# Kernel optimization log

Measured on AMD Instinct MI355X. Metric: run time of the kernel, lower is better.

## Reference

```python
import jax, jax.numpy as jnp
import numpy as np

C_CH, S_DIM, H_DIM, RANK = 256, 16, 128, 8


def setup_inputs() -> dict:
    key = jax.random.key(0)
    k = jax.random.split(key, 6)
    x = jax.random.normal(k[0], (1, C_CH, S_DIM, H_DIM, H_DIM), dtype=jnp.float32)
    # Conv1d(kernel=1, bias=False) weights per rank; kaiming-ish fan_out scaling
    W1 = jax.random.normal(k[1], (RANK, C_CH, C_CH), jnp.float32) * np.sqrt(2.0 / C_CH)
    W2 = jax.random.normal(k[2], (RANK, S_DIM, S_DIM), jnp.float32) * np.sqrt(2.0 / S_DIM)
    W3 = jax.random.normal(k[3], (RANK, H_DIM, H_DIM), jnp.float32) * np.sqrt(2.0 / H_DIM)
    W4 = jax.random.normal(k[4], (RANK, H_DIM, H_DIM), jnp.float32) * np.sqrt(2.0 / H_DIM)
    lam = jnp.ones((RANK,), dtype=jnp.float32)
    return {"x": x, "W1": W1, "W2": W2, "W3": W3, "W4": W4, "lam": lam}


def reference(x, W1, W2, W3, W4, lam):
    # x: (1, c, s, w, h); AdaptiveAvgPool3d(1) on permuted views == global means
    Cv = x.mean(axis=(0, 2, 3, 4))  # (c,)  channel pooling
    Sv = x.mean(axis=(0, 1, 3, 4))  # (s,)
    Hv = x.mean(axis=(0, 1, 2, 3))  # (h,)  last spatial dim
    Wv = x.mean(axis=(0, 1, 2, 4))  # (w,)

    # original detaches softmax(lam) and always uses index 0
    lam_sm = jax.lax.stop_gradient(jax.nn.softmax(lam))
    coef = lam_sm[0]

    # per-rank 1x1 conv + sigmoid == sigmoid(W @ v), batched over rank
    cf = jax.nn.sigmoid(jnp.einsum('rij,j->ri', W1, Cv))  # (r, c)
    sf = jax.nn.sigmoid(jnp.einsum('rij,j->ri', W2, Sv))  # (r, s)
    hf = jax.nn.sigmoid(jnp.einsum('rij,j->ri', W3, Hv))  # (r, h)
    wf = jax.nn.sigmoid(jnp.einsum('rij,j->ri', W4, Wv))  # (r, w)

    # chained bmm with ps=1 == rank-1 outer product, summed over rank
    tensor1 = coef * jnp.einsum('rc,rs,rh,rw->cshw', cf, sf, hf, wf)
    tensor1 = tensor1[None]  # (1, c, s, h, w) matching x layout

    return jnp.concatenate([x, jax.nn.relu(x * tensor1)], axis=1)
```

## Files before the change

kernel.cpp:

```cpp
#include <hip/hip_runtime.h>

typedef float f32x4 __attribute__((ext_vector_type(4)));

#define C_CH 256
#define S_DIM 16
#define HW 128
#define RANK 8
#define NCOPY 16

#define OFF_PC 0
#define OFF_PS 4096
#define OFF_PI 4352
#define OFF_PJ 6400
#define OFF_CF 8448
#define OFF_SF 10496
#define OFF_HF 10624
#define OFF_WF 11648

__global__ __launch_bounds__(256) void k_init(float* __restrict__ ws) {
    int idx = blockIdx.x * 256 + threadIdx.x;
    if (idx < OFF_CF) ws[idx] = 0.f;
}

__global__ __launch_bounds__(256) void k_reduce(const float* __restrict__ x,
                                                float* __restrict__ out,
                                                float* __restrict__ ws) {
    int b = blockIdx.x;
    int c = b >> 2;
    int s0 = (b & 3) * 4;
    int t = threadIdx.x;
    int lane = t & 31;
    int rg = t >> 5;
    int j0 = lane * 4;

    float colacc[4] = {0.f, 0.f, 0.f, 0.f};
    float rowacc[16] = {0.f};
    float tot[4] = {0.f, 0.f, 0.f, 0.f};

    for (int q = 0; q < 4; ++q) {
        size_t slab = (size_t)(b * 4 + q) * 16384;
        const f32x4* xs = reinterpret_cast<const f32x4*>(x + slab);
        f32x4* o1 = reinterpret_cast<f32x4*>(out + slab);
#pragma unroll
        for (int k = 0; k < 16; ++k) {
            f32x4 v = xs[k * 256 + t];
            __builtin_nontemporal_store(v, &o1[k * 256 + t]);
            colacc[0] += v.x; colacc[1] += v.y;
            colacc[2] += v.z; colacc[3] += v.w;
            float s4 = (v.x + v.y) + (v.z + v.w);
            rowacc[k] += s4;
            tot[q] += s4;
        }
    }

    __shared__ float ldsr[128 * 33];
    __shared__ float ldsc[128 * 9];
    __shared__ float ldst[4][4];

#pragma unroll
    for (int k = 0; k < 16; ++k) ldsr[(k * 8 + rg) * 33 + lane] = rowacc[k];
#pragma unroll
    for (int jj = 0; jj < 4; ++jj) ldsc[(j0 + jj) * 9 + rg] = colacc[jj];
#pragma unroll
    for (int q = 0; q < 4; ++q) {
        float v = tot[q];
        for (int d = 32; d > 0; d >>= 1) v += __shfl_down(v, d, 64);
        if ((t & 63) == 0) ldst[t >> 6][q] = v;
    }
    __syncthreads();

    int copy = b & (NCOPY - 1);
    if (t < 128) {
        float rsum = 0.f;
#pragma unroll
        for (int l = 0; l < 32; ++l) rsum += ldsr[t * 33 + l];
        atomicAdd(&ws[OFF_PI + copy * 128 + t], rsum);
    } else {
        int j = t - 128;
        float csum = 0.f;
#pragma unroll
        for (int g = 0; g < 8; ++g) csum += ldsc[j * 9 + g];
        atomicAdd(&ws[OFF_PJ + copy * 128 + j], csum);
    }
    if (t < 4) {
        float sv = ldst[0][t] + ldst[1][t] + ldst[2][t] + ldst[3][t];
        atomicAdd(&ws[OFF_PS + copy * 16 + s0 + t], sv);
    }
    if (t == 8) {
        float cv = 0.f;
#pragma unroll
        for (int w = 0; w < 4; ++w)
#pragma unroll
            for (int q = 0; q < 4; ++q) cv += ldst[w][q];
        atomicAdd(&ws[OFF_PC + copy * 256 + c], cv);
    }
}

__global__ __launch_bounds__(256) void k_factors(const float* __restrict__ W1,
                                                 const float* __restrict__ W2,
                                                 const float* __restrict__ W3,
                                                 const float* __restrict__ W4,
                                                 const float* __restrict__ lam,
                                                 float* __restrict__ ws) {
    __shared__ float mC[256], mS[16], mW[128], mH[128];
    int t = threadIdx.x;
    for (int idx = t; idx < 528; idx += 256) {
        float acc = 0.f;
        if (idx < 256) {
            for (int cp = 0; cp < NCOPY; ++cp) acc += ws[OFF_PC + cp * 256 + idx];
            mC[idx] = acc * (1.f / (S_DIM * 16384.f));
        } else if (idx < 272) {
            int q = idx - 256;
            for (int cp = 0; cp < NCOPY; ++cp) acc += ws[OFF_PS + cp * 16 + q];
            mS[q] = acc * (1.f / (C_CH * 16384.f));
        } else if (idx < 400) {
            int q = idx - 272;
            for (int cp = 0; cp < NCOPY; ++cp) acc += ws[OFF_PI + cp * 128 + q];
            mW[q] = acc * (1.f / (C_CH * S_DIM * 128.f));
        } else {
            int q = idx - 400;
            for (int cp = 0; cp < NCOPY; ++cp) acc += ws[OFF_PJ + cp * 128 + q];
            mH[q] = acc * (1.f / (C_CH * S_DIM * 128.f));
        }
    }
    __syncthreads();

    float m = lam[0];
    for (int r = 1; r < RANK; ++r) m = fmaxf(m, lam[r]);
    float den = 0.f;
    for (int r = 0; r < RANK; ++r) den += expf(lam[r] - m);
    float coef = expf(lam[0] - m) / den;

    int rid = blockIdx.x * 256 + t;
    if (rid < 2048) {
        int r = rid >> 8, i = rid & 255;
        const float* w = W1 + r * 65536 + i * 256;
        float d = 0.f;
        for (int k = 0; k < 256; ++k) d += w[k] * mC[k];
        ws[OFF_CF + rid] = coef / (1.f + expf(-d));
    } else if (rid < 2176) {
        int q = rid - 2048;
        int r = q >> 4, i = q & 15;
        const float* w = W2 + r * 256 + i * 16;
        float d = 0.f;
        for (int k = 0; k < 16; ++k) d += w[k] * mS[k];
        ws[OFF_SF + q] = 1.f / (1.f + expf(-d));
    } else if (rid < 3200) {
        int q = rid - 2176;
        int r = q >> 7, i = q & 127;
        const float* w = W3 + r * 16384 + i * 128;
        float d = 0.f;
        for (int k = 0; k < 128; ++k) d += w[k] * mH[k];
        ws[OFF_HF + q] = 1.f / (1.f + expf(-d));
    } else if (rid < 4224) {
        int q = rid - 3200;
        int r = q >> 7, i = q & 127;
        const float* w = W4 + r * 16384 + i * 128;
        float d = 0.f;
        for (int k = 0; k < 128; ++k) d += w[k] * mW[k];
        ws[OFF_WF + q] = 1.f / (1.f + expf(-d));
    }
}

__global__ __launch_bounds__(256) void k_output(const float* __restrict__ x,
                                                const float* __restrict__ ws,
                                                float* __restrict__ out) {
    int b = blockIdx.x;
    int c = b >> 4, s = b & 15;
    int t = threadIdx.x;

    __shared__ float hb[128 * 8];
    __shared__ float wb[128 * 8];

    const float* cf = ws + OFF_CF;
    const float* sf = ws + OFF_SF;
    const float* hf = ws + OFF_HF;
    const float* wf = ws + OFF_WF;

    for (int idx = t; idx < 1024; idx += 256) {
        int r = idx & 7, p = idx >> 3;
        hb[idx] = hf[r * 128 + p];
        wb[idx] = cf[r * 256 + c] * sf[r * 16 + s] * wf[r * 128 + p];
    }
    __syncthreads();

    int j0 = (t & 31) * 4, rg = t >> 5;
    float wreg[4][8];
#pragma unroll
    for (int jj = 0; jj < 4; ++jj)
#pragma unroll
        for (int r = 0; r < 8; ++r) wreg[jj][r] = wb[(j0 + jj) * 8 + r];

    size_t slab = (size_t)b * 16384;
    const f32x4* xs = reinterpret_cast<const f32x4*>(x + slab);
    f32x4* o2 = reinterpret_cast<f32x4*>(out + (size_t)67108864 + slab);

    for (int k = 0; k < 16; ++k) {
        int i = k * 8 + rg;
        int vidx = i * 32 + (t & 31);
        f32x4 v = xs[vidx];
        float h[8];
#pragma unroll
        for (int r = 0; r < 8; ++r) h[r] = hb[i * 8 + r];
        float t0 = 0.f, t1 = 0.f, t2 = 0.f, t3 = 0.f;
#pragma unroll
        for (int r = 0; r < 8; ++r) {
            t0 += h[r] * wreg[0][r];
            t1 += h[r] * wreg[1][r];
            t2 += h[r] * wreg[2][r];
            t3 += h[r] * wreg[3][r];
        }
        f32x4 y;
        y.x = fmaxf(v.x * t0, 0.f);
        y.y = fmaxf(v.y * t1, 0.f);
        y.z = fmaxf(v.z * t2, 0.f);
        y.w = fmaxf(v.w * t3, 0.f);
        __builtin_nontemporal_store(y, &o2[vidx]);
    }
}

extern "C" void kernel_launch(void* const* d_in, const int* in_sizes, int n_in,
                              void* d_out, int out_size, void* d_ws, size_t ws_size,
                              hipStream_t stream) {
    const float* x   = (const float*)d_in[0];
    const float* W1  = (const float*)d_in[1];
    const float* W2  = (const float*)d_in[2];
    const float* W3  = (const float*)d_in[3];
    const float* W4  = (const float*)d_in[4];
    const float* lam = (const float*)d_in[5];
    float* ws  = (float*)d_ws;
    float* out = (float*)d_out;

    k_init<<<33, 256, 0, stream>>>(ws);
    k_reduce<<<1024, 256, 0, stream>>>(x, out, ws);
    k_factors<<<17, 256, 0, stream>>>(W1, W2, W3, W4, lam, ws);
    k_output<<<4096, 256, 0, stream>>>(x, ws, out);
}
```

Measured before the change: 195.8 us.

## Stage bf16 copy of input in workspace for the gated-output pass

After: 193.2 us (median of 2 runs). No clear change (-1.3%).

```diff
diff --git a/kernel.cpp b/kernel.cpp
--- a/kernel.cpp
+++ b/kernel.cpp
@@ -1,6 +1,7 @@
 #include <hip/hip_runtime.h>
 
 typedef float f32x4 __attribute__((ext_vector_type(4)));
+typedef unsigned short u16x4 __attribute__((ext_vector_type(4)));
 
 #define C_CH 256
 #define S_DIM 16
@@ -16,12 +17,21 @@
 #define OFF_SF 10496
 #define OFF_HF 10624
 #define OFF_WF 11648
+#define OFF_BF 16384
+
+#define BF_WS_BYTES ((size_t)65536 + (size_t)67108864 * 2)
+
+__device__ __forceinline__ unsigned short bf16rne(float f) {
+    unsigned u = __float_as_uint(f);
+    return (unsigned short)((u + 0x7FFFu + ((u >> 16) & 1u)) >> 16);
+}
 
 __global__ __launch_bounds__(256) void k_init(float* __restrict__ ws) {
     int idx = blockIdx.x * 256 + threadIdx.x;
     if (idx < OFF_CF) ws[idx] = 0.f;
 }
 
+template <bool WBF>
 __global__ __launch_bounds__(256) void k_reduce(const float* __restrict__ x,
                                                 float* __restrict__ out,
                                                 float* __restrict__ ws) {
@@ -33,6 +43,9 @@
     int rg = t >> 5;
     int j0 = lane * 4;
 
+    u16x4* bfp = reinterpret_cast<u16x4*>(
+        reinterpret_cast<unsigned short*>(ws + OFF_BF));
+
     float colacc[4] = {0.f, 0.f, 0.f, 0.f};
     float rowacc[16] = {0.f};
     float tot[4] = {0.f, 0.f, 0.f, 0.f};
@@ -41,10 +54,19 @@
         size_t slab = (size_t)(b * 4 + q) * 16384;
         const f32x4* xs = reinterpret_cast<const f32x4*>(x + slab);
         f32x4* o1 = reinterpret_cast<f32x4*>(out + slab);
+        u16x4* bf = bfp + (slab >> 2);
 #pragma unroll
         for (int k = 0; k < 16; ++k) {
-            f32x4 v = xs[k * 256 + t];
+            f32x4 v = __builtin_nontemporal_load(&xs[k * 256 + t]);
             __builtin_nontemporal_store(v, &o1[k * 256 + t]);
+            if (WBF) {
+                u16x4 hv;
+                hv.x = bf16rne(v.x);
+                hv.y = bf16rne(v.y);
+                hv.z = bf16rne(v.z);
+                hv.w = bf16rne(v.w);
+                bf[k * 256 + t] = hv;
+            }
             colacc[0] += v.x; colacc[1] += v.y;
             colacc[2] += v.z; colacc[3] += v.w;
             float s4 = (v.x + v.y) + (v.z + v.w);
@@ -162,9 +184,8 @@
     }
 }
 
-__global__ __launch_bounds__(256) void k_output(const float* __restrict__ x,
-                                                const float* __restrict__ ws,
-                                                float* __restrict__ out) {
+__global__ __launch_bounds__(256) void k_output_bf(const float* __restrict__ ws,
+                                                   float* __restrict__ out) {
     int b = blockIdx.x;
     int c = b >> 4, s = b & 15;
     int t = threadIdx.x;
@@ -191,14 +212,20 @@
 #pragma unroll
         for (int r = 0; r < 8; ++r) wreg[jj][r] = wb[(j0 + jj) * 8 + r];
 
-    size_t slab = (size_t)b * 16384;
-    const f32x4* xs = reinterpret_cast<const f32x4*>(x + slab);
-    f32x4* o2 = reinterpret_cast<f32x4*>(out + (size_t)67108864 + slab);
+    const u16x4* bf = reinterpret_cast<const u16x4*>(
+        reinterpret_cast<const unsigned short*>(ws + OFF_BF));
+    size_t slab4 = (size_t)b * 4096;
+    f32x4* o2 = reinterpret_cast<f32x4*>(out + (size_t)67108864 + (size_t)b * 16384);
 
     for (int k = 0; k < 16; ++k) {
         int i = k * 8 + rg;
         int vidx = i * 32 + (t & 31);
-        f32x4 v = xs[vidx];
+        u16x4 hv = bf[slab4 + vidx];
+        f32x4 v;
+        v.x = __uint_as_float((unsigned)hv.x << 16);
+        v.y = __uint_as_float((unsigned)hv.y << 16);
+        v.z = __uint_as_float((unsigned)hv.z << 16);
+        v.w = __uint_as_float((unsigned)hv.w << 16);
         float h[8];
 #pragma unroll
         for (int r = 0; r < 8; ++r) h[r] = hb[i * 8 + r];
@@ -219,6 +246,63 @@
     }
 }
 
+__global__ __launch_bounds__(256) void k_output_fp(const float* __restrict__ x,
+                                                   const float* __restrict__ ws,
+                                                   float* __restrict__ out) {
+    int b = blockIdx.x;
+    int c = b >> 4, s = b & 15;
+    int t = threadIdx.x;
+
+    __shared__ float hb[128 * 8];
+    __shared__ float wb[128 * 8];
+
+    const float* cf = ws + OFF_CF;
+    const float* sf = ws + OFF_SF;
+    const float* hf = ws + OFF_HF;
+    const float* wf = ws + OFF_WF;
+
+    for (int idx = t; idx < 1024; idx += 256) {
+        int r = idx & 7, p = idx >> 3;
+        hb[idx] = hf[r * 128 + p];
+        wb[idx] = cf[r * 256 + c] * sf[r * 16 + s] * wf[r * 128 + p];
+    }
+    __syncthreads();
+
+    int j0 = (t & 31) * 4, rg = t >> 5;
+    float wreg[4][8];
+#pragma unroll
+    for (int jj = 0; jj < 4; ++jj)
+#pragma unroll
+        for (int r = 0; r < 8; ++r) wreg[jj][r] = wb[(j0 + jj) * 8 + r];
+
+    size_t slab = (size_t)b * 16384;
+    const f32x4* xs = reinterpret_cast<const f32x4*>(x + slab);
+    f32x4* o2 = reinterpret_cast<f32x4*>(out + (size_t)67108864 + slab);
+
+    for (int k = 0; k < 16; ++k) {
+        int i = k * 8 + rg;
+        int vidx = i * 32 + (t & 31);
+        f32x4 v = xs[vidx];
+        float h[8];
+#pragma unroll
+        for (int r = 0; r < 8; ++r) h[r] = hb[i * 8 + r];
+        float t0 = 0.f, t1 = 0.f, t2 = 0.f, t3 = 0.f;
+#pragma unroll
+        for (int r = 0; r < 8; ++r) {
+            t0 += h[r] * wreg[0][r];
+            t1 += h[r] * wreg[1][r];
+            t2 += h[r] * wreg[2][r];
+            t3 += h[r] * wreg[3][r];
+        }
+        f32x4 y;
+        y.x = fmaxf(v.x * t0, 0.f);
+        y.y = fmaxf(v.y * t1, 0.f);
+        y.z = fmaxf(v.z * t2, 0.f);
+        y.w = fmaxf(v.w * t3, 0.f);
+        __builtin_nontemporal_store(y, &o2[vidx]);
+    }
+}
+
 extern "C" void kernel_launch(void* const* d_in, const int* in_sizes, int n_in,
                               void* d_out, int out_size, void* d_ws, size_t ws_size,
                               hipStream_t stream) {
@@ -231,8 +315,16 @@
     float* ws  = (float*)d_ws;
     float* out = (float*)d_out;
 
+    bool use_bf = ws_size >= BF_WS_BYTES;
+
     k_init<<<33, 256, 0, stream>>>(ws);
-    k_reduce<<<1024, 256, 0, stream>>>(x, out, ws);
-    k_factors<<<17, 256, 0, stream>>>(W1, W2, W3, W4, lam, ws);
-    k_output<<<4096, 256, 0, stream>>>(x, ws, out);
-}
+    if (use_bf) {
+        k_reduce<true><<<1024, 256, 0, stream>>>(x, out, ws);
+        k_factors<<<17, 256, 0, stream>>>(W1, W2, W3, W4, lam, ws);
+        k_output_bf<<<4096, 256, 0, stream>>>(ws, out);
+    } else {
+        k_reduce<false><<<1024, 256, 0, stream>>>(x, out, ws);
+        k_factors<<<17, 256, 0, stream>>>(W1, W2, W3, W4, lam, ws);
+        k_output_fp<<<4096, 256, 0, stream>>>(x, ws, out);
+    }
+}
```

## Replace atomic partial sums with per-block partials and drop init kernel

Applied to the files above, without the earlier changes.

Result: slower. 245.5 us (+25.4%).

```diff
diff --git a/kernel.cpp b/kernel.cpp
--- a/kernel.cpp
+++ b/kernel.cpp
@@ -6,28 +6,20 @@
 #define S_DIM 16
 #define HW 128
 #define RANK 8
-#define NCOPY 16
-
-#define OFF_PC 0
-#define OFF_PS 4096
-#define OFF_PI 4352
-#define OFF_PJ 6400
-#define OFF_CF 8448
-#define OFF_SF 10496
-#define OFF_HF 10624
-#define OFF_WF 11648
-
-__global__ __launch_bounds__(256) void k_init(float* __restrict__ ws) {
-    int idx = blockIdx.x * 256 + threadIdx.x;
-    if (idx < OFF_CF) ws[idx] = 0.f;
-}
+
+#define OFF_PI 0
+#define OFF_PJ 131072
+#define OFF_PS 262144
+#define OFF_PC 266240
+#define OFF_CF 267264
+#define OFF_SF 269312
+#define OFF_HF 269440
+#define OFF_WF 270464
 
 __global__ __launch_bounds__(256) void k_reduce(const float* __restrict__ x,
                                                 float* __restrict__ out,
                                                 float* __restrict__ ws) {
     int b = blockIdx.x;
-    int c = b >> 2;
-    int s0 = (b & 3) * 4;
     int t = threadIdx.x;
     int lane = t & 31;
     int rg = t >> 5;
@@ -43,7 +35,7 @@
         f32x4* o1 = reinterpret_cast<f32x4*>(out + slab);
 #pragma unroll
         for (int k = 0; k < 16; ++k) {
-            f32x4 v = xs[k * 256 + t];
+            f32x4 v = __builtin_nontemporal_load(&xs[k * 256 + t]);
             __builtin_nontemporal_store(v, &o1[k * 256 + t]);
             colacc[0] += v.x; colacc[1] += v.y;
             colacc[2] += v.z; colacc[3] += v.w;
@@ -69,22 +61,21 @@
     }
     __syncthreads();
 
-    int copy = b & (NCOPY - 1);
     if (t < 128) {
         float rsum = 0.f;
 #pragma unroll
         for (int l = 0; l < 32; ++l) rsum += ldsr[t * 33 + l];
-        atomicAdd(&ws[OFF_PI + copy * 128 + t], rsum);
+        ws[OFF_PI + b * 128 + t] = rsum;
     } else {
         int j = t - 128;
         float csum = 0.f;
 #pragma unroll
         for (int g = 0; g < 8; ++g) csum += ldsc[j * 9 + g];
-        atomicAdd(&ws[OFF_PJ + copy * 128 + j], csum);
+        ws[OFF_PJ + b * 128 + j] = csum;
     }
     if (t < 4) {
         float sv = ldst[0][t] + ldst[1][t] + ldst[2][t] + ldst[3][t];
-        atomicAdd(&ws[OFF_PS + copy * 16 + s0 + t], sv);
+        ws[OFF_PS + b * 4 + t] = sv;
     }
     if (t == 8) {
         float cv = 0.f;
@@ -92,7 +83,7 @@
         for (int w = 0; w < 4; ++w)
 #pragma unroll
             for (int q = 0; q < 4; ++q) cv += ldst[w][q];
-        atomicAdd(&ws[OFF_PC + copy * 256 + c], cv);
+        ws[OFF_PC + b] = cv;
     }
 }
 
@@ -105,22 +96,43 @@
     __shared__ float mC[256], mS[16], mW[128], mH[128];
     int t = threadIdx.x;
     for (int idx = t; idx < 528; idx += 256) {
-        float acc = 0.f;
         if (idx < 256) {
-            for (int cp = 0; cp < NCOPY; ++cp) acc += ws[OFF_PC + cp * 256 + idx];
-            mC[idx] = acc * (1.f / (S_DIM * 16384.f));
+            const float* pc = ws + OFF_PC + idx * 4;
+            mC[idx] = (pc[0] + pc[1] + pc[2] + pc[3]) * (1.f / (S_DIM * 16384.f));
         } else if (idx < 272) {
-            int q = idx - 256;
-            for (int cp = 0; cp < NCOPY; ++cp) acc += ws[OFF_PS + cp * 16 + q];
-            mS[q] = acc * (1.f / (C_CH * 16384.f));
+            int s = idx - 256;
+            int a = s >> 2, d = s & 3;
+            const float* ps = ws + OFF_PS;
+            float a0 = 0.f, a1 = 0.f, a2 = 0.f, a3 = 0.f;
+            for (int k = 0; k < 256; k += 4) {
+                a0 += ps[((k + 0) * 4 + a) * 4 + d];
+                a1 += ps[((k + 1) * 4 + a) * 4 + d];
+                a2 += ps[((k + 2) * 4 + a) * 4 + d];
+                a3 += ps[((k + 3) * 4 + a) * 4 + d];
+            }
+            mS[s] = ((a0 + a1) + (a2 + a3)) * (1.f / (C_CH * 16384.f));
         } else if (idx < 400) {
             int q = idx - 272;
-            for (int cp = 0; cp < NCOPY; ++cp) acc += ws[OFF_PI + cp * 128 + q];
-            mW[q] = acc * (1.f / (C_CH * S_DIM * 128.f));
+            const float* pi = ws + OFF_PI + q;
+            float a0 = 0.f, a1 = 0.f, a2 = 0.f, a3 = 0.f;
+            for (int bb = 0; bb < 1024; bb += 4) {
+                a0 += pi[(bb + 0) * 128];
+                a1 += pi[(bb + 1) * 128];
+                a2 += pi[(bb + 2) * 128];
+                a3 += pi[(bb + 3) * 128];
+            }
+            mW[q] = ((a0 + a1) + (a2 + a3)) * (1.f / (C_CH * S_DIM * 128.f));
         } else {
             int q = idx - 400;
-            for (int cp = 0; cp < NCOPY; ++cp) acc += ws[OFF_PJ + cp * 128 + q];
-            mH[q] = acc * (1.f / (C_CH * S_DIM * 128.f));
+            const float* pj = ws + OFF_PJ + q;
+            float a0 = 0.f, a1 = 0.f, a2 = 0.f, a3 = 0.f;
+            for (int bb = 0; bb < 1024; bb += 4) {
+                a0 += pj[(bb + 0) * 128];
+                a1 += pj[(bb + 1) * 128];
+                a2 += pj[(bb + 2) * 128];
+                a3 += pj[(bb + 3) * 128];
+            }
+            mH[q] = ((a0 + a1) + (a2 + a3)) * (1.f / (C_CH * S_DIM * 128.f));
         }
     }
     __syncthreads();
@@ -198,7 +210,7 @@
     for (int k = 0; k < 16; ++k) {
         int i = k * 8 + rg;
         int vidx = i * 32 + (t & 31);
-        f32x4 v = xs[vidx];
+        f32x4 v = __builtin_nontemporal_load(&xs[vidx]);
         float h[8];
 #pragma unroll
         for (int r = 0; r < 8; ++r) h[r] = hb[i * 8 + r];
@@ -231,7 +243,6 @@
     float* ws  = (float*)d_ws;
     float* out = (float*)d_out;
 
-    k_init<<<33, 256, 0, stream>>>(ws);
     k_reduce<<<1024, 256, 0, stream>>>(x, out, ws);
     k_factors<<<17, 256, 0, stream>>>(W1, W2, W3, W4, lam, ws);
     k_output<<<4096, 256, 0, stream>>>(x, ws, out);
```
